# Kernel tuning notes

Hardware: AMD Instinct MI355X
Metric: run time of the kernel (lower is better)

Reference implementation:

```python
import jax, jax.numpy as jnp
import numpy as np

B, N, F_IN, F_OUT, E = 2, 8192, 64, 64, 262144
ALPHA = 0.2  # LeakyReLU negative slope


def setup_inputs() -> dict:
    key = jax.random.key(0)
    k1, k2, k3, k4, k5 = jax.random.split(key, 5)
    h = jax.random.normal(k1, (B, N, F_IN), dtype=jnp.float32)
    edge_index = jax.random.randint(k2, (2, E), 0, N, dtype=jnp.int64)
    edge_weight = jax.random.uniform(k3, (E,), dtype=jnp.float32)
    # torch Linear(in,out,bias=False): weight shape (out, in)
    lim_w = float(np.sqrt(1.0 / F_IN))
    W = jax.random.uniform(k4, (F_OUT, F_IN), minval=-lim_w, maxval=lim_w, dtype=jnp.float32)
    # xavier_uniform on (2*out, 1)
    lim_a = float(np.sqrt(6.0 / (2 * F_OUT + 1)))
    a = jax.random.uniform(k5, (2 * F_OUT, 1), minval=-lim_a, maxval=lim_a, dtype=jnp.float32)
    return {"h": h, "W": W, "a": a, "edge_index": edge_index, "edge_weight": edge_weight}


def reference(h, W, a, edge_index, edge_weight):
    src, dst = edge_index[0], edge_index[1]

    def single(hb):  # hb: (N, F_IN)
        Wh = hb @ W.T  # (N, F_OUT)
        edge_h = jnp.concatenate([Wh[src], Wh[dst]], axis=1)  # (E, 2*F_OUT)
        e = jax.nn.leaky_relu((edge_h @ a)[:, 0], negative_slope=ALPHA)  # (E,)
        e = e * edge_weight
        # dense N x N attention, zeros treated as masked (faithful to source)
        attn = jnp.zeros((N, N), dtype=Wh.dtype).at[src, dst].set(e)
        mask = attn == 0
        attn = jnp.where(mask, -jnp.inf, attn)
        attn = jax.nn.softmax(attn, axis=1)
        attn = jnp.where(mask, 0.0, attn)
        h_prime = attn @ Wh  # (N, F_OUT)
        return jax.nn.elu(h_prime)  # concat=True path

    return jax.vmap(single)(h)
```

## Files before the change

### kernel.cpp

```cpp
#include <hip/hip_runtime.h>
#include <hip/hip_bf16.h>
#include <math.h>

#define NN     8192
#define FDIM   64
#define EDGES  262144
#define BATCH  2
#define ALPHA  0.2f

#define NB     256
#define SRCB   32
#define BCAP   1280
#define ROWCAP 128

#define OFF_WH   0u
#define OFF_S1   4194304u
#define OFF_S2   4259840u
#define OFF_CNT  4325376u
#define OFF_CRS  4326400u

__global__ __launch_bounds__(1024) void stage1_kernel(
    const float* __restrict__ h, const float* __restrict__ W,
    const float* __restrict__ a, const int* __restrict__ ei,
    float* __restrict__ Wh, float* __restrict__ s1, float* __restrict__ s2,
    int* __restrict__ cnt, uint2* __restrict__ coarse) {
  __shared__ float sW[64 * 65];
  __shared__ float sH[64 * 64];
  __shared__ int bhist[NB];
  __shared__ int bbase[NB];
  int tid = threadIdx.x, lane = tid & 63, w = tid >> 6;
  int blk = blockIdx.x;

  int e = blk * 1024 + tid;
  int s = ei[e], d = ei[EDGES + e];
  int g = s >> 5;
  if (tid < NB) bhist[tid] = 0;
  __syncthreads();
  int rank = atomicAdd(&bhist[g], 1);
  __syncthreads();
  int baseReg = 0;
  if (tid < NB) baseReg = atomicAdd(&cnt[tid], bhist[tid]);

  for (int i = tid; i < 4096; i += 1024) sW[(i >> 6) * 65 + (i & 63)] = W[i];
  int rr = lane >> 4, c4 = lane & 15;
  int nn0 = blk * 64 + w * 4;
  *(float4*)(sH + (w * 4 + rr) * 64 + c4 * 4) =
      *(const float4*)(h + (size_t)(nn0 + rr) * 64 + c4 * 4);
  __syncthreads();

  const float* wp = sW + lane * 65;
  const float* hp = sH + (w * 4) * 64;
  float acc[4] = {0.f, 0.f, 0.f, 0.f};
#pragma unroll 8
  for (int k = 0; k < 64; ++k) {
    float wv = wp[k];
    acc[0] += hp[k] * wv;
    acc[1] += hp[64 + k] * wv;
    acc[2] += hp[128 + k] * wv;
    acc[3] += hp[192 + k] * wv;
  }
  float a1 = a[lane], a2 = a[64 + lane];
#pragma unroll
  for (int r = 0; r < 4; ++r) {
    int nn = nn0 + r;
    Wh[(size_t)nn * 64 + lane] = acc[r];
    float p1 = acc[r] * a1, p2 = acc[r] * a2;
#pragma unroll
    for (int off = 32; off; off >>= 1) {
      p1 += __shfl_xor(p1, off, 64);
      p2 += __shfl_xor(p2, off, 64);
    }
    if (lane == 0) { s1[nn] = p1; s2[nn] = p2; }
  }

  if (tid < NB) bbase[tid] = baseReg;
  __syncthreads();
  int pos = bbase[g] + rank;
  if (pos < BCAP)
    coarse[g * BCAP + pos] = make_uint2(((unsigned)e << 13) | (unsigned)d, (unsigned)s);
}

__global__ __launch_bounds__(1024) void stage2_kernel(
    const float* __restrict__ ew, const float* __restrict__ s1,
    const float* __restrict__ s2, const int* __restrict__ cnt,
    const uint2* __restrict__ coarse, const float* __restrict__ Wh,
    float* __restrict__ out) {
  __shared__ uint2 grp[BCAP];
  __shared__ int rhist[SRCB];
  __shared__ int roffs[SRCB];
  int tid = threadIdx.x, lane = tid & 63, w = tid >> 6;
  int blk = blockIdx.x;
  int xcd = blk & 7;
  int b = xcd >> 2;
  int g = (blk >> 3) * 4 + (xcd & 3);
  int T = cnt[g]; if (T > BCAP) T = BCAP;
  const float* s1b = s1 + b * NN;
  const float* s2b = s2 + b * NN;
  if (tid < SRCB) rhist[tid] = 0;
  __syncthreads();

  unsigned mpk[2]; float mv[2]; int msl[2], mrk[2]; bool mok[2];
#pragma unroll
  for (int j = 0; j < 2; ++j) {
    int i = tid + j * 1024;
    mok[j] = (i < T);
    mpk[j] = 0; mv[j] = 0.f; msl[j] = 0; mrk[j] = 0;
    if (mok[j]) {
      uint2 E = coarse[g * BCAP + i];
      int dst = (int)(E.x & 0x1FFFu);
      int eid = (int)(E.x >> 13);
      int src = (int)E.y;
      float x = s1b[src] + s2b[dst];
      float val = (x > 0.f ? x : ALPHA * x) * ew[eid];
      mpk[j] = E.x; mv[j] = val; msl[j] = src & (SRCB - 1);
      mrk[j] = atomicAdd(&rhist[msl[j]], 1);
    }
  }
  __syncthreads();
  if (tid < SRCB) {
    int c = rhist[tid];
    int x = c;
#pragma unroll
    for (int off = 1; off < SRCB; off <<= 1) {
      int y = __shfl_up(x, off, 64);
      if (tid >= off) x += y;
    }
    roffs[tid] = x - c;
  }
  __syncthreads();
#pragma unroll
  for (int j = 0; j < 2; ++j)
    if (mok[j]) grp[roffs[msl[j]] + mrk[j]] = make_uint2(mpk[j], __float_as_uint(mv[j]));
  __syncthreads();

  const float* Whb = Wh + (size_t)b * NN * FDIM;
  int fg = lane & 15, es = lane >> 4;
  for (int q = 0; q < 2; ++q) {
    int slo = w * 2 + q;
    int beg = roffs[slo];
    int deg = rhist[slo];
    int n = g * SRCB + slo;
    float4 r4 = make_float4(0.f, 0.f, 0.f, 0.f);
    if (deg > 0) {
      float inv;
      if (deg <= 64) {
        unsigned k0 = 0; float v0 = 0.f;
        if (lane < deg) { uint2 E = grp[beg + lane]; k0 = E.x; v0 = __uint_as_float(E.y); }
        for (int j = 0; j < deg; ++j) {
          unsigned q2 = __shfl(k0, j, 64);
          if ((((q2 ^ k0) & 0x1FFFu) == 0u) & (q2 > k0)) v0 = 0.f;
        }
        float m = (v0 != 0.f) ? v0 : -INFINITY;
#pragma unroll
        for (int off = 32; off; off >>= 1) m = fmaxf(m, __shfl_xor(m, off, 64));
        float p = (v0 != 0.f) ? expf(v0 - m) : 0.f;
        float sum = p;
#pragma unroll
        for (int off = 32; off; off >>= 1) sum += __shfl_xor(sum, off, 64);
        inv = (sum > 0.f) ? 1.f / sum : 0.f;
        if (lane < deg) grp[beg + lane].y = __float_as_uint(p);
      } else {
        int dg = deg > ROWCAP ? ROWCAP : deg;
        deg = dg;
        unsigned k0 = 0, k1 = 0; float v0 = 0.f, v1 = 0.f;
        { uint2 E = grp[beg + lane]; k0 = E.x; v0 = __uint_as_float(E.y); }
        if (lane + 64 < dg) { uint2 E = grp[beg + lane + 64]; k1 = E.x; v1 = __uint_as_float(E.y); }
        for (int j = 0; j < 64; ++j) {
          unsigned q2 = __shfl(k0, j, 64);
          if ((((q2 ^ k0) & 0x1FFFu) == 0u) & (q2 > k0)) v0 = 0.f;
          if ((((q2 ^ k1) & 0x1FFFu) == 0u) & (q2 > k1)) v1 = 0.f;
        }
        for (int j = 0; j < dg - 64; ++j) {
          unsigned q2 = __shfl(k1, j, 64);
          if ((((q2 ^ k0) & 0x1FFFu) == 0u) & (q2 > k0)) v0 = 0.f;
          if ((((q2 ^ k1) & 0x1FFFu) == 0u) & (q2 > k1)) v1 = 0.f;
        }
        float m = fmaxf((v0 != 0.f) ? v0 : -INFINITY, (v1 != 0.f) ? v1 : -INFINITY);
#pragma unroll
        for (int off = 32; off; off >>= 1) m = fmaxf(m, __shfl_xor(m, off, 64));
        float p0 = (v0 != 0.f) ? expf(v0 - m) : 0.f;
        float p1 = (v1 != 0.f) ? expf(v1 - m) : 0.f;
        float sum = p0 + p1;
#pragma unroll
        for (int off = 32; off; off >>= 1) sum += __shfl_xor(sum, off, 64);
        inv = (sum > 0.f) ? 1.f / sum : 0.f;
        grp[beg + lane].y = __float_as_uint(p0);
        if (lane + 64 < dg) grp[beg + lane + 64].y = __float_as_uint(p1);
      }
      float4 acc = make_float4(0.f, 0.f, 0.f, 0.f);
      for (int kk = 0; kk < deg; kk += 8) {
#pragma unroll
        for (int u = 0; u < 2; ++u) {
          int k = kk + u * 4 + es;
          int kc = k < deg ? k : deg - 1;
          uint2 E = grp[beg + kc];
          float p = (k < deg) ? __uint_as_float(E.y) : 0.f;
          const float4* src4 = (const float4*)(Whb + (E.x & 0x1FFFu) * 64) + fg;
          float4 v = *src4;
          acc.x += p * v.x; acc.y += p * v.y; acc.z += p * v.z; acc.w += p * v.w;
        }
      }
#pragma unroll
      for (int off = 16; off <= 32; off <<= 1) {
        acc.x += __shfl_xor(acc.x, off, 64);
        acc.y += __shfl_xor(acc.y, off, 64);
        acc.z += __shfl_xor(acc.z, off, 64);
        acc.w += __shfl_xor(acc.w, off, 64);
      }
      r4.x = acc.x * inv; r4.y = acc.y * inv; r4.z = acc.z * inv; r4.w = acc.w * inv;
    }
    if (es == 0) {
      r4.x = r4.x > 0.f ? r4.x : expm1f(r4.x);
      r4.y = r4.y > 0.f ? r4.y : expm1f(r4.y);
      r4.z = r4.z > 0.f ? r4.z : expm1f(r4.z);
      r4.w = r4.w > 0.f ? r4.w : expm1f(r4.w);
      *((float4*)(out + ((size_t)b * NN + n) * 64) + fg) = r4;
    }
  }
}

extern "C" void kernel_launch(void* const* d_in, const int* in_sizes, int n_in,
                              void* d_out, int out_size, void* d_ws, size_t ws_size,
                              hipStream_t stream) {
  const float* h  = (const float*)d_in[0];
  const float* W  = (const float*)d_in[1];
  const float* a  = (const float*)d_in[2];
  const int*   ei = (const int*)d_in[3];
  const float* ew = (const float*)d_in[4];
  float* out = (float*)d_out;

  char* ws = (char*)d_ws;
  float* Wh     = (float*)(ws + OFF_WH);
  float* s1     = (float*)(ws + OFF_S1);
  float* s2     = (float*)(ws + OFF_S2);
  int*   cnt    = (int*)(ws + OFF_CNT);
  uint2* coarse = (uint2*)(ws + OFF_CRS);

  hipMemsetAsync(cnt, 0, NB * sizeof(int), stream);
  stage1_kernel<<<256, 1024, 0, stream>>>(h, W, a, ei, Wh, s1, s2, cnt, coarse);
  stage2_kernel<<<BATCH * NB, 1024, 0, stream>>>(ew, s1, s2, cnt, coarse, Wh, out);
}
```

Measured before the change: 110.4 us.

## Replace global atomic bucketing with per-block local sort and offset table

```diff
diff --git a/kernel.cpp b/kernel.cpp
--- a/kernel.cpp
+++ b/kernel.cpp
@@ -13,33 +13,49 @@
 #define BCAP   1280
 #define ROWCAP 128
 
-#define OFF_WH   0u
-#define OFF_S1   4194304u
-#define OFF_S2   4259840u
-#define OFF_CNT  4325376u
-#define OFF_CRS  4326400u
+#define OFF_WH    0u
+#define OFF_S1    4194304u
+#define OFF_S2    4259840u
+#define OFF_OFFS  4325376u
+#define OFF_CRS   4456448u
 
 __global__ __launch_bounds__(1024) void stage1_kernel(
     const float* __restrict__ h, const float* __restrict__ W,
     const float* __restrict__ a, const int* __restrict__ ei,
     float* __restrict__ Wh, float* __restrict__ s1, float* __restrict__ s2,
-    int* __restrict__ cnt, uint2* __restrict__ coarse) {
+    unsigned short* __restrict__ offsT, uint2* __restrict__ coarse) {
   __shared__ float sW[64 * 65];
   __shared__ float sH[64 * 64];
-  __shared__ int bhist[NB];
-  __shared__ int bbase[NB];
+  __shared__ int hist[NB];
+  __shared__ int offs[NB];
   int tid = threadIdx.x, lane = tid & 63, w = tid >> 6;
   int blk = blockIdx.x;
 
   int e = blk * 1024 + tid;
   int s = ei[e], d = ei[EDGES + e];
   int g = s >> 5;
-  if (tid < NB) bhist[tid] = 0;
-  __syncthreads();
-  int rank = atomicAdd(&bhist[g], 1);
-  __syncthreads();
-  int baseReg = 0;
-  if (tid < NB) baseReg = atomicAdd(&cnt[tid], bhist[tid]);
+  if (tid < NB) hist[tid] = 0;
+  __syncthreads();
+  int rank = atomicAdd(&hist[g], 1);
+  __syncthreads();
+  if (tid < 64) {
+    int i0 = tid * 4;
+    int c0 = hist[i0], c1 = hist[i0 + 1], c2 = hist[i0 + 2], c3 = hist[i0 + 3];
+    int sum = c0 + c1 + c2 + c3;
+    int x = sum;
+#pragma unroll
+    for (int off = 1; off < 64; off <<= 1) {
+      int y = __shfl_up(x, off, 64);
+      if (tid >= off) x += y;
+    }
+    int ex = x - sum;
+    offs[i0] = ex; offs[i0 + 1] = ex + c0;
+    offs[i0 + 2] = ex + c0 + c1; offs[i0 + 3] = ex + c0 + c1 + c2;
+  }
+  __syncthreads();
+  coarse[blk * 1024 + offs[g] + rank] =
+      make_uint2(((unsigned)e << 13) | (unsigned)d, (unsigned)s);
+  if (tid < NB) offsT[tid * 256 + blk] = (unsigned short)offs[tid];
 
   for (int i = tid; i < 4096; i += 1024) sW[(i >> 6) * 65 + (i & 63)] = W[i];
   int rr = lane >> 4, c4 = lane & 15;
@@ -72,20 +88,16 @@
     }
     if (lane == 0) { s1[nn] = p1; s2[nn] = p2; }
   }
-
-  if (tid < NB) bbase[tid] = baseReg;
-  __syncthreads();
-  int pos = bbase[g] + rank;
-  if (pos < BCAP)
-    coarse[g * BCAP + pos] = make_uint2(((unsigned)e << 13) | (unsigned)d, (unsigned)s);
 }
 
 __global__ __launch_bounds__(1024) void stage2_kernel(
     const float* __restrict__ ew, const float* __restrict__ s1,
-    const float* __restrict__ s2, const int* __restrict__ cnt,
+    const float* __restrict__ s2, const unsigned short* __restrict__ offsT,
     const uint2* __restrict__ coarse, const float* __restrict__ Wh,
     float* __restrict__ out) {
   __shared__ uint2 grp[BCAP];
+  __shared__ int dstBase[257];
+  __shared__ int srcPos[256];
   __shared__ int rhist[SRCB];
   __shared__ int roffs[SRCB];
   int tid = threadIdx.x, lane = tid & 63, w = tid >> 6;
@@ -93,11 +105,34 @@
   int xcd = blk & 7;
   int b = xcd >> 2;
   int g = (blk >> 3) * 4 + (xcd & 3);
-  int T = cnt[g]; if (T > BCAP) T = BCAP;
   const float* s1b = s1 + b * NN;
   const float* s2b = s2 + b * NN;
   if (tid < SRCB) rhist[tid] = 0;
-  __syncthreads();
+
+  if (tid < 256) {
+    int lo = offsT[g * 256 + tid];
+    int hi = (g == 255) ? 1024 : offsT[(g + 1) * 256 + tid];
+    srcPos[tid] = tid * 1024 + lo;
+    dstBase[tid] = hi - lo;
+  }
+  __syncthreads();
+  if (tid < 64) {
+    int i0 = tid * 4;
+    int c0 = dstBase[i0], c1 = dstBase[i0 + 1], c2 = dstBase[i0 + 2], c3 = dstBase[i0 + 3];
+    int sum = c0 + c1 + c2 + c3;
+    int x = sum;
+#pragma unroll
+    for (int off = 1; off < 64; off <<= 1) {
+      int y = __shfl_up(x, off, 64);
+      if (tid >= off) x += y;
+    }
+    int ex = x - sum;
+    dstBase[i0] = ex; dstBase[i0 + 1] = ex + c0;
+    dstBase[i0 + 2] = ex + c0 + c1; dstBase[i0 + 3] = ex + c0 + c1 + c2;
+    if (tid == 63) dstBase[256] = x;
+  }
+  __syncthreads();
+  int T = dstBase[256]; if (T > BCAP) T = BCAP;
 
   unsigned mpk[2]; float mv[2]; int msl[2], mrk[2]; bool mok[2];
 #pragma unroll
@@ -106,7 +141,14 @@
     mok[j] = (i < T);
     mpk[j] = 0; mv[j] = 0.f; msl[j] = 0; mrk[j] = 0;
     if (mok[j]) {
-      uint2 E = coarse[g * BCAP + i];
+      int lo = 0, hi = 255;
+#pragma unroll
+      for (int st = 0; st < 8; ++st) {
+        int mid = (lo + hi + 1) >> 1;
+        if (dstBase[mid] <= i) lo = mid; else hi = mid - 1;
+      }
+      int c = lo, jj = i - dstBase[c];
+      uint2 E = coarse[srcPos[c] + jj];
       int dst = (int)(E.x & 0x1FFFu);
       int eid = (int)(E.x >> 13);
       int src = (int)E.y;
@@ -188,16 +230,20 @@
         if (lane + 64 < dg) grp[beg + lane + 64].y = __float_as_uint(p1);
       }
       float4 acc = make_float4(0.f, 0.f, 0.f, 0.f);
-      for (int kk = 0; kk < deg; kk += 8) {
-#pragma unroll
-        for (int u = 0; u < 2; ++u) {
+      for (int kk = 0; kk < deg; kk += 32) {
+        float4 vv[8]; float pp[8];
+#pragma unroll
+        for (int u = 0; u < 8; ++u) {
           int k = kk + u * 4 + es;
           int kc = k < deg ? k : deg - 1;
           uint2 E = grp[beg + kc];
-          float p = (k < deg) ? __uint_as_float(E.y) : 0.f;
-          const float4* src4 = (const float4*)(Whb + (E.x & 0x1FFFu) * 64) + fg;
-          float4 v = *src4;
-          acc.x += p * v.x; acc.y += p * v.y; acc.z += p * v.z; acc.w += p * v.w;
+          pp[u] = (k < deg) ? __uint_as_float(E.y) : 0.f;
+          vv[u] = *((const float4*)(Whb + (E.x & 0x1FFFu) * 64) + fg);
+        }
+#pragma unroll
+        for (int u = 0; u < 8; ++u) {
+          acc.x += pp[u] * vv[u].x; acc.y += pp[u] * vv[u].y;
+          acc.z += pp[u] * vv[u].z; acc.w += pp[u] * vv[u].w;
         }
       }
 #pragma unroll
@@ -230,13 +276,12 @@
   float* out = (float*)d_out;
 
   char* ws = (char*)d_ws;
-  float* Wh     = (float*)(ws + OFF_WH);
-  float* s1     = (float*)(ws + OFF_S1);
-  float* s2     = (float*)(ws + OFF_S2);
-  int*   cnt    = (int*)(ws + OFF_CNT);
-  uint2* coarse = (uint2*)(ws + OFF_CRS);
-
-  hipMemsetAsync(cnt, 0, NB * sizeof(int), stream);
-  stage1_kernel<<<256, 1024, 0, stream>>>(h, W, a, ei, Wh, s1, s2, cnt, coarse);
-  stage2_kernel<<<BATCH * NB, 1024, 0, stream>>>(ew, s1, s2, cnt, coarse, Wh, out);
+  float*          Wh    = (float*)(ws + OFF_WH);
+  float*          s1    = (float*)(ws + OFF_S1);
+  float*          s2    = (float*)(ws + OFF_S2);
+  unsigned short* offsT = (unsigned short*)(ws + OFF_OFFS);
+  uint2*          coarse = (uint2*)(ws + OFF_CRS);
+
+  stage1_kernel<<<256, 1024, 0, stream>>>(h, W, a, ei, Wh, s1, s2, offsT, coarse);
+  stage2_kernel<<<BATCH * NB, 1024, 0, stream>>>(ew, s1, s2, offsT, coarse, Wh, out);
 }
```

After: 107.3 us. -2.8%, faster.
